# Performance work log

Hardware: AMD Instinct MI355X
Metric: run time of the kernel (lower is better)

## Reference

```python
import jax, jax.numpy as jnp
import numpy as np

N_NODES = 100000
N_EDGES = 1600000
D_IN = 64
D_OUT = 64
K_PLUS = 3
ALPHA = 0.5
EXPONENT = -0.25


def _dir_norm_edge_weights(row, col, n, exponent):
    # directed_norm: D_out^exp A D_in^exp, zero-degree -> 0 weight
    ones = jnp.ones(row.shape[0], dtype=jnp.float32)
    out_deg = jax.ops.segment_sum(ones, row, num_segments=n)
    in_deg = jax.ops.segment_sum(ones, col, num_segments=n)
    out_inv = jnp.where(out_deg > 0, jnp.power(jnp.maximum(out_deg, 1.0), exponent), 0.0)
    in_inv = jnp.where(in_deg > 0, jnp.power(jnp.maximum(in_deg, 1.0), exponent), 0.0)
    return out_inv[row] * in_inv[col]


def _spmm(w, x, out_idx, gather_idx, n):
    # y[out_idx] += w * x[gather_idx]
    return jax.ops.segment_sum(w[:, None] * x[gather_idx], out_idx, num_segments=n)


def setup_inputs() -> dict:
    key = jax.random.key(0)
    ks = jax.random.split(key, 7)
    x_real = jax.random.normal(ks[0], (N_NODES, D_IN), dtype=jnp.float32)
    x_imag = jax.random.normal(ks[1], (N_NODES, D_IN), dtype=jnp.float32)
    edge_index = jax.random.randint(ks[2], (2, N_EDGES), 0, N_NODES, dtype=jnp.int32)
    s = 1.0 / np.sqrt(D_IN)
    W_real = jax.random.normal(ks[3], (K_PLUS, D_OUT, D_IN), dtype=jnp.float32) * s
    b_real = jax.random.normal(ks[4], (K_PLUS, D_OUT), dtype=jnp.float32) * s
    W_imag = jax.random.normal(ks[5], (K_PLUS, D_OUT, D_IN), dtype=jnp.float32) * s
    b_imag = jax.random.normal(ks[6], (K_PLUS, D_OUT), dtype=jnp.float32) * s
    return {"x_real": x_real, "x_imag": x_imag, "edge_index": edge_index,
            "W_real": W_real, "b_real": b_real, "W_imag": W_imag, "b_imag": b_imag}


def reference(x_real, x_imag, edge_index, W_real, b_real, W_imag, b_imag):
    n = x_real.shape[0]
    row, col = edge_index[0], edge_index[1]
    # adj_norm edge weights; adj_t_norm weights are identical scalars per edge
    # (in/out degrees swap under transpose), only the scatter direction differs.
    w = _dir_norm_edge_weights(row, col, n, EXPONENT)

    y_real = _spmm(w, x_real, row, col, n)    # adj_norm @ x_real
    y_imag = _spmm(w, x_imag, row, col, n)    # adj_norm @ x_imag
    y_real_t = _spmm(w, x_real, col, row, n)  # adj_t_norm @ x_real
    y_imag_t = _spmm(w, x_imag, col, row, n)  # adj_t_norm @ x_imag

    def lin_r(y):  # [K, N, O] per-order real linear
        return jnp.einsum('nd,kod->kno', y, W_real) + b_real[:, None, :]

    def lin_i(y):
        return jnp.einsum('nd,kod->kno', y, W_imag) + b_imag[:, None, :]

    coeffs = (0.5 ** jnp.arange(K_PLUS, dtype=jnp.float32))[:, None, None]  # exp penalty, i=0 -> 1

    lr_yr, li_yr = lin_r(y_real), lin_i(y_real)
    lr_yi, li_yi = lin_r(y_imag), lin_i(y_imag)
    lr_yrt, li_yrt = lin_r(y_real_t), lin_i(y_real_t)
    lr_yit, li_yit = lin_r(y_imag_t), lin_i(y_imag_t)

    sum_real_s2d = jnp.sum((lr_yr - li_yi) * coeffs, axis=0)
    sum_imag_s2d = jnp.sum((li_yr + lr_yi) * coeffs, axis=0)
    sum_real_d2s = jnp.sum((lr_yrt - li_yit) * coeffs, axis=0)
    # NOTE: faithful to original source, which uses y_real (not y_real_t) here.
    sum_imag_d2s = jnp.sum((li_yr + lr_yit) * coeffs, axis=0)

    total_real = ALPHA * sum_real_s2d + (1.0 - ALPHA) * sum_real_d2s
    total_imag = ALPHA * sum_imag_s2d + (1.0 - ALPHA) * sum_imag_d2s
    return total_real, total_imag
```

## Files before the change

### kernel.cpp

```cpp
#include <hip/hip_runtime.h>
#include <hip/hip_fp16.h>


constexpr int D = 64;
constexpr int SB = 256;
constexpr int G1 = 256;

__device__ __forceinline__ float2 h2_to_f2(uint p) {
  __half2 h = *(__half2*)&p;
  return __half22float2(h);
}


__global__ __launch_bounds__(256) void part_count(
    const int* __restrict__ row, const int* __restrict__ col,
    int* __restrict__ hout, int* __restrict__ hin, int E, int NBUK, int CH) {
  __shared__ int ho[256], hi_[256];
  int t = threadIdx.x, g = blockIdx.x;
  ho[t] = 0;
  hi_[t] = 0;
  __syncthreads();
  int e0 = g * CH, e1 = min(E, e0 + CH);
  for (int e = e0 + t; e < e1; e += 256) {
    atomicAdd(&ho[row[e] >> 9], 1);
    atomicAdd(&hi_[col[e] >> 9], 1);
  }
  __syncthreads();
  if (t < NBUK) {
    hout[t * G1 + g] = ho[t];
    hin[t * G1 + g] = hi_[t];
  }
}

__global__ __launch_bounds__(256) void part_scatter(
    const int* __restrict__ row, const int* __restrict__ col,
    const int* __restrict__ hout, const int* __restrict__ hin,
    uint* __restrict__ pout, uint* __restrict__ pin, int E, int NBUK, int CH) {
  __shared__ int co[256], ci[256];
  int t = threadIdx.x, g = blockIdx.x;
  if (t < NBUK) {
    co[t] = hout[t * G1 + g];
    ci[t] = hin[t * G1 + g];
  }
  __syncthreads();
  int e0 = g * CH, e1 = min(E, e0 + CH);
  for (int e = e0 + t; e < e1; e += 256) {
    int r = row[e], c = col[e];
    int po = atomicAdd(&co[r >> 9], 1);
    pout[po] = ((uint)(r & 511) << 17) | (uint)c;
    int pi = atomicAdd(&ci[c >> 9], 1);
    pin[pi] = ((uint)(c & 511) << 17) | (uint)r;
  }
}

__global__ __launch_bounds__(256) void bucket_degree(
    const uint* __restrict__ pout, const uint* __restrict__ pin,
    const int* __restrict__ hout, const int* __restrict__ hin,
    int* __restrict__ deg_out, int* __restrict__ deg_in, int E, int NBUK, int N) {
  const uint* p = blockIdx.y ? pin : pout;
  const int* h = blockIdx.y ? hin : hout;
  int* deg = blockIdx.y ? deg_in : deg_out;
  __shared__ int ld[512];
  int t = threadIdx.x, b = blockIdx.x;
  ld[t] = 0;
  ld[t + 256] = 0;
  __syncthreads();
  int s = h[b * G1];
  int e = (b + 1 < NBUK) ? h[(b + 1) * G1] : E;
  for (int j = s + t; j < e; j += 256) atomicAdd(&ld[p[j] >> 17], 1);
  __syncthreads();
  int n0 = (b << 9) + t;
  if (n0 < N) deg[n0] = ld[t];
  if (n0 + 256 < N) deg[n0 + 256] = ld[t + 256];
}

__global__ __launch_bounds__(256) void bucket_fill(
    const uint* __restrict__ pout, const uint* __restrict__ pin,
    const int* __restrict__ hout, const int* __restrict__ hin,
    const int* __restrict__ ofs_out, const int* __restrict__ ofs_in,
    uint* __restrict__ idx_out, uint* __restrict__ idx_in, int E, int NBUK, int N) {
  const uint* p = blockIdx.y ? pin : pout;
  const int* h = blockIdx.y ? hin : hout;
  const int* ofs = blockIdx.y ? ofs_in : ofs_out;
  uint* idx = blockIdx.y ? idx_in : idx_out;
  __shared__ int cur[512];
  int t = threadIdx.x, b = blockIdx.x;
  int n0 = (b << 9) + t;
  cur[t] = (n0 < N) ? ofs[n0] : 0;
  cur[t + 256] = (n0 + 256 < N) ? ofs[n0 + 256] : 0;
  __syncthreads();
  int s = h[b * G1];
  int e = (b + 1 < NBUK) ? h[(b + 1) * G1] : E;
  for (int j = s + t; j < e; j += 256) {
    uint pk = p[j];
    int pos = atomicAdd(&cur[pk >> 17], 1);
    idx[pos] = pk & 0x1FFFFu;
  }
}


__global__ __launch_bounds__(SB) void bsum_kernel(
    const int* __restrict__ a0, const int* __restrict__ a1,
    int* __restrict__ bsum, int n, int NB) {
  const int* a = blockIdx.y ? a1 : a0;
  int i = blockIdx.x * SB + threadIdx.x;
  int d = (i < n) ? a[i] : 0;
#pragma unroll
  for (int m = 1; m < 64; m <<= 1) d += __shfl_xor(d, m);
  __shared__ int ws[SB / 64];
  if ((threadIdx.x & 63) == 0) ws[threadIdx.x >> 6] = d;
  __syncthreads();
  if (threadIdx.x == 0) {
    int s = 0;
#pragma unroll
    for (int w = 0; w < SB / 64; ++w) s += ws[w];
    bsum[blockIdx.y * NB + blockIdx.x] = s;
  }
}

__global__ __launch_bounds__(1024) void bscan_kernel(int* __restrict__ bsum, int NB) {
  __shared__ int s0[1024], s1[1024];
  int t = threadIdx.x;
  int o0 = (t < NB) ? bsum[t] : 0;
  int o1 = (t < NB) ? bsum[NB + t] : 0;
  s0[t] = o0;
  s1[t] = o1;
  __syncthreads();
  for (int off = 1; off < 1024; off <<= 1) {
    int v0 = (t >= off) ? s0[t - off] : 0;
    int v1 = (t >= off) ? s1[t - off] : 0;
    __syncthreads();
    s0[t] += v0;
    s1[t] += v1;
    __syncthreads();
  }
  if (t < NB) {
    bsum[t] = s0[t] - o0;
    bsum[NB + t] = s1[t] - o1;
  }
}

__global__ __launch_bounds__(SB) void gfin_kernel(
    int* __restrict__ h0, int* __restrict__ h1,
    const int* __restrict__ bsum, int n, int NB) {
  int* h = blockIdx.y ? h1 : h0;
  int base = bsum[blockIdx.y * NB + blockIdx.x];
  int lane = threadIdx.x & 63, wv = threadIdx.x >> 6;
  int i = blockIdx.x * SB + threadIdx.x;
  int d = (i < n) ? h[i] : 0;
  int sc = d;
#pragma unroll
  for (int off = 1; off < 64; off <<= 1) {
    int v = __shfl_up(sc, off);
    if (lane >= off) sc += v;
  }
  __shared__ int ws[SB / 64];
  if (lane == 63) ws[wv] = sc;
  __syncthreads();
  int wbase = 0;
#pragma unroll
  for (int w = 0; w < SB / 64; ++w)
    if (w < wv) wbase += ws[w];
  if (i < n) h[i] = base + wbase + (sc - d);
}

__global__ __launch_bounds__(SB) void sfin_kernel(
    const int* __restrict__ deg_out, const int* __restrict__ deg_in,
    const int* __restrict__ bsum,
    int* __restrict__ ofs_out, int* __restrict__ ofs_in,
    float* __restrict__ inv_out, float* __restrict__ inv_in, int N, int NB) {
  const int* deg = blockIdx.y ? deg_in : deg_out;
  int* ofs = blockIdx.y ? ofs_in : ofs_out;
  float* inv = blockIdx.y ? inv_in : inv_out;
  int base = bsum[blockIdx.y * NB + blockIdx.x];
  int lane = threadIdx.x & 63, wv = threadIdx.x >> 6;
  int i = blockIdx.x * SB + threadIdx.x;
  int d = (i < N) ? deg[i] : 0;
  int sc = d;
#pragma unroll
  for (int off = 1; off < 64; off <<= 1) {
    int v = __shfl_up(sc, off);
    if (lane >= off) sc += v;
  }
  __shared__ int ws[SB / 64];
  if (lane == 63) ws[wv] = sc;
  __syncthreads();
  int wbase = 0;
#pragma unroll
  for (int w = 0; w < SB / 64; ++w)
    if (w < wv) wbase += ws[w];
  if (i < N) {
    ofs[i] = base + wbase + (sc - d);
    inv[i] = d > 0 ? rsqrtf(sqrtf((float)d)) : 0.0f;
  }
  if (i == N - 1) ofs[N] = base + wbase + sc;
}


__global__ void pack_kernel(const float* __restrict__ xr, const float* __restrict__ xi,
                            const float* __restrict__ inv_out, const float* __restrict__ inv_in,
                            uint* __restrict__ xout_p, uint* __restrict__ xin_p, int total4) {
  int i = blockIdx.x * blockDim.x + threadIdx.x;
  if (i < total4) {
    int n = i >> 4;
    float4 a = ((const float4*)xr)[i];
    float4 b = ((const float4*)xi)[i];
    float io = inv_out[n], ii = inv_in[n];
    __half2 h;
    uint4 o, p;
    h = __floats2half2_rn(io * a.x, io * b.x); o.x = *(uint*)&h;
    h = __floats2half2_rn(io * a.y, io * b.y); o.y = *(uint*)&h;
    h = __floats2half2_rn(io * a.z, io * b.z); o.z = *(uint*)&h;
    h = __floats2half2_rn(io * a.w, io * b.w); o.w = *(uint*)&h;
    h = __floats2half2_rn(ii * a.x, ii * b.x); p.x = *(uint*)&h;
    h = __floats2half2_rn(ii * a.y, ii * b.y); p.y = *(uint*)&h;
    h = __floats2half2_rn(ii * a.z, ii * b.z); p.z = *(uint*)&h;
    h = __floats2half2_rn(ii * a.w, ii * b.w); p.w = *(uint*)&h;
    ((uint4*)xout_p)[i] = o;
    ((uint4*)xin_p)[i] = p;
  }
}

__global__ void weights_kernel(const float* __restrict__ Wr, const float* __restrict__ br,
                               const float* __restrict__ Wi, const float* __restrict__ bi,
                               uint* __restrict__ Wh, float* __restrict__ cR,
                               float* __restrict__ cI) {
  int i = blockIdx.x * blockDim.x + threadIdx.x;
  if (i < 4096) {
    int o = i >> 6, d = i & 63;
    float wr = Wr[i] + 0.5f * Wr[4096 + i] + 0.25f * Wr[8192 + i];
    float wi = Wi[i] + 0.5f * Wi[4096 + i] + 0.25f * Wi[8192 + i];
    __half2 h = __floats2half2_rn(wr, wi);
    Wh[d * 64 + o] = *(uint*)&h;
    if (i < 64) {
      float brv = br[i] + 0.5f * br[64 + i] + 0.25f * br[128 + i];
      float biv = bi[i] + 0.5f * bi[64 + i] + 0.25f * bi[128 + i];
      cR[i] = brv - biv;
      cI[i] = brv + biv;
    }
  }
}

__global__ __launch_bounds__(256) void gather_kernel(
    const uint4* __restrict__ xout4, const uint4* __restrict__ xin4,
    const uint* __restrict__ idx_out, const uint* __restrict__ idx_in,
    const int* __restrict__ ofs_out, const int* __restrict__ ofs_in,
    const float* __restrict__ inv_out, const float* __restrict__ inv_in,
    const uint* __restrict__ Wh, const float* __restrict__ cR, const float* __restrict__ cI,
    float* __restrict__ out_real, float* __restrict__ out_imag, int N) {
  __shared__ uint sW[4096];
  __shared__ float4 sV[4][64];
  for (int i = threadIdx.x; i < 4096; i += 256) sW[i] = Wh[i];
  __syncthreads();
  int wv = __builtin_amdgcn_readfirstlane(threadIdx.x >> 6);
  int lane = threadIdx.x & 63;
  int sub = lane >> 4;
  int q = lane & 15;
  float cRv = cR[lane], cIv = cI[lane];
  float4* mv = &sV[wv][0];
  int wid = blockIdx.x * 4 + wv;
  int nw = gridDim.x * 4;
  for (int n = wid; n < N; n += nw) {
    float4 u1 = {0, 0, 0, 0}, s1 = {0, 0, 0, 0};
    float4 v2 = {0, 0, 0, 0}, s2 = {0, 0, 0, 0};
#define ACC(P, U, S)                                          \
  {                                                           \
    float2 a0 = h2_to_f2((P).x), a1 = h2_to_f2((P).y);        \
    float2 a2 = h2_to_f2((P).z), a3 = h2_to_f2((P).w);        \
    U.x += a0.x; S.x += a0.y; U.y += a1.x; S.y += a1.y;       \
    U.z += a2.x; S.z += a2.y; U.w += a3.x; S.w += a3.y;       \
  }
    {
      int lo = ofs_out[n], hi = ofs_out[n + 1];
      int len8 = (hi - lo) & ~7;
      int j = lo;
      for (; j < lo + len8; j += 8) {
        uint4 p0 = xin4[(size_t)idx_out[j + sub] * 16 + q];
        uint4 p1 = xin4[(size_t)idx_out[j + 4 + sub] * 16 + q];
        ACC(p0, u1, s1);
        ACC(p1, u1, s1);
      }
      for (; j < hi; j += 4) {
        if (j + sub < hi) {
          uint4 p0 = xin4[(size_t)idx_out[j + sub] * 16 + q];
          ACC(p0, u1, s1);
        }
      }
    }
    {
      int lo = ofs_in[n], hi = ofs_in[n + 1];
      int len8 = (hi - lo) & ~7;
      int j = lo;
      for (; j < lo + len8; j += 8) {
        uint4 p0 = xout4[(size_t)idx_in[j + sub] * 16 + q];
        uint4 p1 = xout4[(size_t)idx_in[j + 4 + sub] * 16 + q];
        ACC(p0, v2, s2);
        ACC(p1, v2, s2);
      }
      for (; j < hi; j += 4) {
        if (j + sub < hi) {
          uint4 p0 = xout4[(size_t)idx_in[j + sub] * 16 + q];
          ACC(p0, v2, s2);
        }
      }
    }
#undef ACC
#pragma unroll
    for (int m = 16; m < 64; m <<= 1) {
      u1.x += __shfl_xor(u1.x, m); u1.y += __shfl_xor(u1.y, m);
      u1.z += __shfl_xor(u1.z, m); u1.w += __shfl_xor(u1.w, m);
      s1.x += __shfl_xor(s1.x, m); s1.y += __shfl_xor(s1.y, m);
      s1.z += __shfl_xor(s1.z, m); s1.w += __shfl_xor(s1.w, m);
      v2.x += __shfl_xor(v2.x, m); v2.y += __shfl_xor(v2.y, m);
      v2.z += __shfl_xor(v2.z, m); v2.w += __shfl_xor(v2.w, m);
      s2.x += __shfl_xor(s2.x, m); s2.y += __shfl_xor(s2.y, m);
      s2.z += __shfl_xor(s2.z, m); s2.w += __shfl_xor(s2.w, m);
    }
    float io = inv_out[n], ii = inv_in[n];
    if (sub == 0) {
      float4 uu = {io * u1.x, io * u1.y, io * u1.z, io * u1.w};
      float4 vv = {ii * v2.x, ii * v2.y, ii * v2.z, ii * v2.w};
      float4 ss = {io * s1.x + ii * s2.x, io * s1.y + ii * s2.y,
                   io * s1.z + ii * s2.z, io * s1.w + ii * s2.w};
      mv[4 * q + 0] = make_float4(0.5f * (uu.x + vv.x), 0.5f * ss.x, uu.x, 0.0f);
      mv[4 * q + 1] = make_float4(0.5f * (uu.y + vv.y), 0.5f * ss.y, uu.y, 0.0f);
      mv[4 * q + 2] = make_float4(0.5f * (uu.z + vv.z), 0.5f * ss.z, uu.z, 0.0f);
      mv[4 * q + 3] = make_float4(0.5f * (uu.w + vv.w), 0.5f * ss.w, uu.w, 0.0f);
    }
    float accR = cRv, accI = cIv;
#pragma unroll 4
    for (int d = 0; d < 64; ++d) {
      float4 pv = mv[d];
      float2 w2 = h2_to_f2(sW[d * 64 + lane]);
      accR += pv.x * w2.x - pv.y * w2.y;
      accI += pv.y * w2.x + pv.z * w2.y;
    }
    out_real[(size_t)n * D + lane] = accR;
    out_imag[(size_t)n * D + lane] = accI;
  }
}

extern "C" void kernel_launch(void* const* d_in, const int* in_sizes, int n_in,
                              void* d_out, int out_size, void* d_ws, size_t ws_size,
                              hipStream_t stream) {
  const float* x_real = (const float*)d_in[0];
  const float* x_imag = (const float*)d_in[1];
  const int* edge = (const int*)d_in[2];
  const float* W_real = (const float*)d_in[3];
  const float* b_real = (const float*)d_in[4];
  const float* W_imag = (const float*)d_in[5];
  const float* b_imag = (const float*)d_in[6];

  const int N = in_sizes[0] / D;
  const int E = in_sizes[2] / 2;
  const int* row = edge;
  const int* col = edge + E;

  const int NBUK = (N + 511) >> 9;
  const int CH = (E + G1 - 1) / G1;
  const int L = NBUK * G1;
  const int GB = (L + SB - 1) / SB;
  const int NB = (N + SB - 1) / SB;

  uint* xout_p   = (uint*)d_ws;
  uint* xin_p    = xout_p + (size_t)N * D;
  uint* pout     = xin_p + (size_t)N * D;
  uint* pin      = pout + E;
  uint* idx_out  = pin + E;
  uint* idx_in   = idx_out + E;
  int* hout      = (int*)(idx_in + E);
  int* hin       = hout + L;
  int* gbs       = hin + L;
  int* deg_out   = gbs + 2 * GB;
  int* deg_in    = deg_out + N;
  int* ofs_out   = deg_in + N;
  int* ofs_in    = ofs_out + N + 1;
  float* inv_out = (float*)(ofs_in + N + 1);
  float* inv_in  = inv_out + N;
  uint* Wh       = (uint*)(inv_in + N);
  float* cR      = (float*)(Wh + 4096);
  float* cI      = cR + 64;
  int* bsum      = (int*)(cI + 64);

  float* out_real = (float*)d_out;
  float* out_imag = out_real + (size_t)N * D;

  weights_kernel<<<16, 256, 0, stream>>>(W_real, b_real, W_imag, b_imag, Wh, cR, cI);

  part_count<<<G1, 256, 0, stream>>>(row, col, hout, hin, E, NBUK, CH);
  bsum_kernel<<<dim3(GB, 2), SB, 0, stream>>>(hout, hin, gbs, L, GB);
  bscan_kernel<<<1, 1024, 0, stream>>>(gbs, GB);
  gfin_kernel<<<dim3(GB, 2), SB, 0, stream>>>(hout, hin, gbs, L, GB);
  part_scatter<<<G1, 256, 0, stream>>>(row, col, hout, hin, pout, pin, E, NBUK, CH);

  bucket_degree<<<dim3(NBUK, 2), 256, 0, stream>>>(pout, pin, hout, hin,
                                                   deg_out, deg_in, E, NBUK, N);
  bsum_kernel<<<dim3(NB, 2), SB, 0, stream>>>(deg_out, deg_in, bsum, N, NB);
  bscan_kernel<<<1, 1024, 0, stream>>>(bsum, NB);
  sfin_kernel<<<dim3(NB, 2), SB, 0, stream>>>(deg_out, deg_in, bsum, ofs_out, ofs_in,
                                              inv_out, inv_in, N, NB);

  pack_kernel<<<(N * 16 + 255) / 256, 256, 0, stream>>>(x_real, x_imag, inv_out, inv_in,
                                                        xout_p, xin_p, N * 16);
  bucket_fill<<<dim3(NBUK, 2), 256, 0, stream>>>(pout, pin, hout, hin, ofs_out, ofs_in,
                                                 idx_out, idx_in, E, NBUK, N);
  gather_kernel<<<4096, 256, 0, stream>>>((const uint4*)xout_p, (const uint4*)xin_p,
                                          idx_out, idx_in, ofs_out, ofs_in,
                                          inv_out, inv_in, Wh, cR, cI,
                                          out_real, out_imag, N);
}
```

Before: 387.1 us.

## Split dense projection out of gather into MFMA fp16 GEMM kernel

The gather kernel no longer does the per-node 64x64 scalar dot products from LDS. It now writes a packed fp16 A matrix (three 64-wide segments per node) to workspace, and a new GEMM kernel multiplies it with prearranged B fragments using 16x16x32 f16 MFMA, adding biases on output. This moves the linear layer onto matrix cores and removes LDS weight staging from the gather. In exchange it adds an extra round trip through global memory for the intermediate, one more launch, and fp16 rounding of the aggregated features. The workspace layout is reshuffled so Apack reuses the partition buffers.

Result: faster. 348.1 us (-10.1%).

```diff
diff --git a/kernel.cpp b/kernel.cpp
--- a/kernel.cpp
+++ b/kernel.cpp
@@ -5,6 +5,9 @@
 constexpr int D = 64;
 constexpr int SB = 256;
 constexpr int G1 = 256;
+
+typedef _Float16 f16x8 __attribute__((ext_vector_type(8)));
+typedef float f32x4 __attribute__((ext_vector_type(4)));
 
 __device__ __forceinline__ float2 h2_to_f2(uint p) {
   __half2 h = *(__half2*)&p;
@@ -241,23 +244,41 @@
   }
 }
 
+__global__ __launch_bounds__(256) void bprep_kernel(
+    const uint* __restrict__ Wh, uint4* __restrict__ Bfrag) {
+  int t = blockIdx.x * blockDim.x + threadIdx.x;
+  if (t >= 2048) return;
+  int lane = t & 63, fr = t >> 6;
+  int mat = fr >> 4, kt = (fr >> 2) & 3, nt = fr & 3;
+  int o = (lane & 15) + 16 * nt;
+  int k0 = 8 * (lane >> 4) + 32 * kt;
+  uint wbits[4];
+#pragma unroll
+  for (int jj = 0; jj < 4; ++jj) {
+    float v[2];
+#pragma unroll
+    for (int s = 0; s < 2; ++s) {
+      int k = k0 + 2 * jj + s;
+      uint wv_ = Wh[(k & 63) * 64 + o];
+      float2 wrwi = h2_to_f2(wv_);
+      v[s] = (k < 64) ? wrwi.x : (mat ? wrwi.y : -wrwi.y);
+    }
+    __half2 hh = __floats2half2_rn(v[0], v[1]);
+    wbits[jj] = *(uint*)&hh;
+  }
+  Bfrag[t] = make_uint4(wbits[0], wbits[1], wbits[2], wbits[3]);
+}
+
 __global__ __launch_bounds__(256) void gather_kernel(
     const uint4* __restrict__ xout4, const uint4* __restrict__ xin4,
     const uint* __restrict__ idx_out, const uint* __restrict__ idx_in,
     const int* __restrict__ ofs_out, const int* __restrict__ ofs_in,
     const float* __restrict__ inv_out, const float* __restrict__ inv_in,
-    const uint* __restrict__ Wh, const float* __restrict__ cR, const float* __restrict__ cI,
-    float* __restrict__ out_real, float* __restrict__ out_imag, int N) {
-  __shared__ uint sW[4096];
-  __shared__ float4 sV[4][64];
-  for (int i = threadIdx.x; i < 4096; i += 256) sW[i] = Wh[i];
-  __syncthreads();
-  int wv = __builtin_amdgcn_readfirstlane(threadIdx.x >> 6);
+    uint* __restrict__ Apack, int N) {
+  int wv = threadIdx.x >> 6;
   int lane = threadIdx.x & 63;
   int sub = lane >> 4;
   int q = lane & 15;
-  float cRv = cR[lane], cIv = cI[lane];
-  float4* mv = &sV[wv][0];
   int wid = blockIdx.x * 4 + wv;
   int nw = gridDim.x * 4;
   for (int n = wid; n < N; n += nw) {
@@ -316,27 +337,79 @@
       s2.x += __shfl_xor(s2.x, m); s2.y += __shfl_xor(s2.y, m);
       s2.z += __shfl_xor(s2.z, m); s2.w += __shfl_xor(s2.w, m);
     }
-    float io = inv_out[n], ii = inv_in[n];
     if (sub == 0) {
-      float4 uu = {io * u1.x, io * u1.y, io * u1.z, io * u1.w};
-      float4 vv = {ii * v2.x, ii * v2.y, ii * v2.z, ii * v2.w};
-      float4 ss = {io * s1.x + ii * s2.x, io * s1.y + ii * s2.y,
-                   io * s1.z + ii * s2.z, io * s1.w + ii * s2.w};
-      mv[4 * q + 0] = make_float4(0.5f * (uu.x + vv.x), 0.5f * ss.x, uu.x, 0.0f);
-      mv[4 * q + 1] = make_float4(0.5f * (uu.y + vv.y), 0.5f * ss.y, uu.y, 0.0f);
-      mv[4 * q + 2] = make_float4(0.5f * (uu.z + vv.z), 0.5f * ss.z, uu.z, 0.0f);
-      mv[4 * q + 3] = make_float4(0.5f * (uu.w + vv.w), 0.5f * ss.w, uu.w, 0.0f);
-    }
-    float accR = cRv, accI = cIv;
-#pragma unroll 4
-    for (int d = 0; d < 64; ++d) {
-      float4 pv = mv[d];
-      float2 w2 = h2_to_f2(sW[d * 64 + lane]);
-      accR += pv.x * w2.x - pv.y * w2.y;
-      accI += pv.y * w2.x + pv.z * w2.y;
-    }
-    out_real[(size_t)n * D + lane] = accR;
-    out_imag[(size_t)n * D + lane] = accI;
+      float io = inv_out[n], ii = inv_in[n];
+      float4 uu = make_float4(io * u1.x, io * u1.y, io * u1.z, io * u1.w);
+      float4 vv = make_float4(ii * v2.x, ii * v2.y, ii * v2.z, ii * v2.w);
+      float4 ss = make_float4(io * s1.x + ii * s2.x, io * s1.y + ii * s2.y,
+                              io * s1.z + ii * s2.z, io * s1.w + ii * s2.w);
+      uint* base = Apack + (size_t)n * 96 + 2 * q;
+      __half2 h;
+      uint2 w;
+      h = __floats2half2_rn(0.5f * (uu.x + vv.x), 0.5f * (uu.y + vv.y)); w.x = *(uint*)&h;
+      h = __floats2half2_rn(0.5f * (uu.z + vv.z), 0.5f * (uu.w + vv.w)); w.y = *(uint*)&h;
+      *(uint2*)base = w;
+      h = __floats2half2_rn(0.5f * ss.x, 0.5f * ss.y); w.x = *(uint*)&h;
+      h = __floats2half2_rn(0.5f * ss.z, 0.5f * ss.w); w.y = *(uint*)&h;
+      *(uint2*)(base + 32) = w;
+      h = __floats2half2_rn(uu.x, uu.y); w.x = *(uint*)&h;
+      h = __floats2half2_rn(uu.z, uu.w); w.y = *(uint*)&h;
+      *(uint2*)(base + 64) = w;
+    }
+  }
+}
+
+__global__ __launch_bounds__(256) void gemm_kernel(
+    const ushort* __restrict__ Apack, const uint4* __restrict__ Bfrag,
+    const float* __restrict__ cR, const float* __restrict__ cI,
+    float* __restrict__ out_real, float* __restrict__ out_imag, int N) {
+  __shared__ uint4 sB[2048];
+  for (int i = threadIdx.x; i < 2048; i += 256) sB[i] = Bfrag[i];
+  __syncthreads();
+  int lane = threadIdx.x & 63, wv = threadIdx.x >> 6;
+  int l15 = lane & 15, l4 = lane >> 4;
+  float bR[4], bI[4];
+#pragma unroll
+  for (int nt = 0; nt < 4; ++nt) {
+    bR[nt] = cR[l15 + 16 * nt];
+    bI[nt] = cI[l15 + 16 * nt];
+  }
+  int tiles = (N + 15) >> 4;
+  int gw = blockIdx.x * 4 + wv, nw = gridDim.x * 4;
+  for (int tt = gw; tt < tiles; tt += nw) {
+    int n0 = tt << 4;
+    int arow = min(n0 + l15, N - 1);
+    const ushort* ap = Apack + (size_t)arow * 192 + 8 * l4;
+    f16x8 a[6];
+#pragma unroll
+    for (int kt = 0; kt < 6; ++kt) a[kt] = *(const f16x8*)(ap + 32 * kt);
+    f32x4 cr[4], ci[4];
+#pragma unroll
+    for (int nt = 0; nt < 4; ++nt) {
+      cr[nt] = (f32x4){0.f, 0.f, 0.f, 0.f};
+      ci[nt] = (f32x4){0.f, 0.f, 0.f, 0.f};
+    }
+#pragma unroll
+    for (int kt = 0; kt < 4; ++kt) {
+#pragma unroll
+      for (int nt = 0; nt < 4; ++nt) {
+        f16x8 b0 = *(const f16x8*)&sB[(kt * 4 + nt) * 64 + lane];
+        cr[nt] = __builtin_amdgcn_mfma_f32_16x16x32_f16(a[kt], b0, cr[nt], 0, 0, 0);
+        f16x8 b1 = *(const f16x8*)&sB[(16 + kt * 4 + nt) * 64 + lane];
+        ci[nt] = __builtin_amdgcn_mfma_f32_16x16x32_f16(a[kt + 2], b1, ci[nt], 0, 0, 0);
+      }
+    }
+#pragma unroll
+    for (int nt = 0; nt < 4; ++nt) {
+#pragma unroll
+      for (int r = 0; r < 4; ++r) {
+        int node = n0 + 4 * l4 + r;
+        if (node < N) {
+          out_real[(size_t)node * 64 + l15 + 16 * nt] = cr[nt][r] + bR[nt];
+          out_imag[(size_t)node * 64 + l15 + 16 * nt] = ci[nt][r] + bI[nt];
+        }
+      }
+    }
   }
 }
 
@@ -364,11 +437,13 @@
 
   uint* xout_p   = (uint*)d_ws;
   uint* xin_p    = xout_p + (size_t)N * D;
-  uint* pout     = xin_p + (size_t)N * D;
+  uint* idx_out  = xin_p + (size_t)N * D;
+  uint* idx_in   = idx_out + E;
+  uint* Apack    = idx_in + E;
+  uint* pout     = Apack;
   uint* pin      = pout + E;
-  uint* idx_out  = pin + E;
-  uint* idx_in   = idx_out + E;
-  int* hout      = (int*)(idx_in + E);
+  uint4* Bfrag   = (uint4*)(Apack + (size_t)N * 96);
+  int* hout      = (int*)(Bfrag + 2048);
   int* hin       = hout + L;
   int* gbs       = hin + L;
   int* deg_out   = gbs + 2 * GB;
@@ -386,6 +461,7 @@
   float* out_imag = out_real + (size_t)N * D;
 
   weights_kernel<<<16, 256, 0, stream>>>(W_real, b_real, W_imag, b_imag, Wh, cR, cI);
+  bprep_kernel<<<8, 256, 0, stream>>>(Wh, Bfrag);
 
   part_count<<<G1, 256, 0, stream>>>(row, col, hout, hin, E, NBUK, CH);
   bsum_kernel<<<dim3(GB, 2), SB, 0, stream>>>(hout, hin, gbs, L, GB);
@@ -406,6 +482,7 @@
                                                  idx_out, idx_in, E, NBUK, N);
   gather_kernel<<<4096, 256, 0, stream>>>((const uint4*)xout_p, (const uint4*)xin_p,
                                           idx_out, idx_in, ofs_out, ofs_in,
-                                          inv_out, inv_in, Wh, cR, cI,
-                                          out_real, out_imag, N);
-}
+                                          inv_out, inv_in, Apack, N);
+  gemm_kernel<<<512, 256, 0, stream>>>((const ushort*)Apack, Bfrag, cR, cI,
+                                       out_real, out_imag, N);
+}
```
